# Kernel tuning notes

Measured on AMD Instinct MI355X. Metric: run time of the kernel, lower is better.

Reference implementation:

```python
import jax, jax.numpy as jnp
import numpy as np
from jax import lax

IMG_DIM = 512
D_MODEL = 768
N_LAYER = 12
D_INNER = 2 * D_MODEL          # 1536
D_STATE = 16
D_CONV = 4
DT_RANK = (D_MODEL + 15) // 16 # 48
BATCH = 4
SEQ = 256


def setup_inputs() -> dict:
    key = jax.random.key(0)
    ks = jax.random.split(key, 16)
    s = 0.02
    inp = {
        "frames_rep": jax.random.normal(ks[0], (BATCH, SEQ, IMG_DIM), jnp.float32),
        "fproj_w": jax.random.normal(ks[1], (IMG_DIM, D_MODEL), jnp.float32) * s,
        "fproj_b": jnp.zeros((D_MODEL,), jnp.float32),
        "norm_w": jnp.ones((N_LAYER, D_MODEL), jnp.float32),
        "in_w": jax.random.normal(ks[2], (N_LAYER, D_MODEL, 2 * D_INNER), jnp.float32) * s,
        "conv_w": jax.random.normal(ks[3], (N_LAYER, D_INNER, D_CONV), jnp.float32) * s,
        "conv_b": jnp.zeros((N_LAYER, D_INNER), jnp.float32),
        "xproj_w": jax.random.normal(ks[4], (N_LAYER, D_INNER, DT_RANK + 2 * D_STATE), jnp.float32) * s,
        "dt_w": jax.random.normal(ks[5], (N_LAYER, DT_RANK, D_INNER), jnp.float32) * s,
        "dt_b": jnp.full((N_LAYER, D_INNER), -2.0, jnp.float32),  # softplus(-2)~0.13
        "A_log": jnp.broadcast_to(jnp.log(jnp.arange(1, D_STATE + 1, dtype=jnp.float32)), (N_LAYER, D_INNER, D_STATE)) * jnp.ones((N_LAYER, D_INNER, 1)),
        "D_param": jnp.ones((N_LAYER, D_INNER), jnp.float32),
        "out_w": jax.random.normal(ks[6], (N_LAYER, D_INNER, D_MODEL), jnp.float32) * s,
        "normf_w": jnp.ones((D_MODEL,), jnp.float32),
    }
    return inp


def _rmsnorm(x, w, eps=1e-5):
    return x * lax.rsqrt(jnp.mean(x * x, axis=-1, keepdims=True) + eps) * w


def _mamba_layer(x, in_w, conv_w, conv_b, xproj_w, dt_w, dt_b, A_log, D_param, out_w):
    # x: (B, L, D_MODEL)
    B, L, _ = x.shape
    xz = x @ in_w                                  # (B, L, 2*di)
    xi, res = jnp.split(xz, 2, axis=-1)            # each (B, L, di)
    # depthwise causal conv over time
    xc = jnp.transpose(xi, (0, 2, 1))              # (B, di, L)
    xc = lax.conv_general_dilated(
        xc, conv_w[:, None, :], (1,), [(D_CONV - 1, 0)],
        feature_group_count=D_INNER)
    xi = jax.nn.silu(jnp.transpose(xc + conv_b[None, :, None], (0, 2, 1)))
    # input-dependent SSM parameters
    x_dbl = xi @ xproj_w                           # (B, L, dt_rank + 2n)
    delta = x_dbl[..., :DT_RANK]
    Bm = x_dbl[..., DT_RANK:DT_RANK + D_STATE]     # (B, L, n)
    Cm = x_dbl[..., DT_RANK + D_STATE:]            # (B, L, n)
    delta = jax.nn.softplus(delta @ dt_w + dt_b)   # (B, L, di)
    A = -jnp.exp(A_log)                            # (di, n)
    deltaA = jnp.exp(delta[..., None] * A)                               # (B, L, di, n)
    deltaBu = delta[..., None] * Bm[:, :, None, :] * xi[..., None]       # (B, L, di, n)

    def step(h, inp):
        dA, dBu, c = inp
        h = dA * h + dBu                           # (B, di, n)
        y = jnp.einsum('bdn,bn->bd', h, c)
        return h, y

    xs = (deltaA.transpose(1, 0, 2, 3), deltaBu.transpose(1, 0, 2, 3), Cm.transpose(1, 0, 2))
    h0 = jnp.zeros((B, D_INNER, D_STATE), x.dtype)
    _, ys = lax.scan(step, h0, xs)                 # (L, B, di)
    y = ys.transpose(1, 0, 2) + xi * D_param
    y = y * jax.nn.silu(res)
    return y @ out_w                               # (B, L, D_MODEL)


def reference(frames_rep, fproj_w, fproj_b, norm_w, in_w, conv_w, conv_b,
              xproj_w, dt_w, dt_b, A_log, D_param, out_w, normf_w):
    h = jax.nn.relu(frames_rep @ fproj_w + fproj_b)       # (B, L, D_MODEL)
    for i in range(N_LAYER):
        h = h + _mamba_layer(_rmsnorm(h, norm_w[i]), in_w[i], conv_w[i], conv_b[i],
                             xproj_w[i], dt_w[i], dt_b[i], A_log[i], D_param[i], out_w[i])
    return _rmsnorm(h, normf_w)
```

## Files before the change

kernel.cpp:

```cpp
#include <hip/hip_runtime.h>
#include <hip/hip_bf16.h>
#include <cmath>

#define IMG_DIM 512
#define D_MODEL 768
#define N_LAYER 12
#define D_INNER 1536
#define D_STATE 16
#define D_CONV 4
#define DT_RANK 48
#define BATCH 4
#define SEQ 256
#define M_TOK (BATCH * SEQ)
#define XPROJ_N (DT_RANK + 2 * D_STATE)
#define KSPLIT 8
#define NCHUNK 16
#define CLEN 16
#define LOG2E 1.4426950408889634f

typedef __attribute__((ext_vector_type(8))) short bf16x8;
typedef __attribute__((ext_vector_type(4))) float f32x4;
typedef __hip_bfloat16 bf16;

__device__ __forceinline__ float softplus_f(float v) {
    return v > 20.f ? v : log1pf(expf(v));
}
__device__ __forceinline__ float b2f(bf16 v) { return __bfloat162float(v); }

__global__ __launch_bounds__(256) void wcvt_t_k(
    const float* __restrict__ W, bf16* __restrict__ WT, int K, int N)
{
    __shared__ float tile[32][33];
    W  += (size_t)blockIdx.z * K * N;
    WT += (size_t)blockIdx.z * K * N;
    const int tx = threadIdx.x & 31;
    const int ty4 = (threadIdx.x >> 5) * 4;
    const int n0 = blockIdx.x * 32, k0 = blockIdx.y * 32;
    #pragma unroll
    for (int r = 0; r < 4; ++r)
        tile[ty4 + r][tx] = (n0 + tx < N)
            ? W[(size_t)(k0 + ty4 + r) * N + n0 + tx] : 0.f;
    __syncthreads();
    #pragma unroll
    for (int r = 0; r < 4; ++r)
        if (n0 + ty4 + r < N)
            WT[(size_t)(n0 + ty4 + r) * K + k0 + tx] =
                __float2bfloat16(tile[tx][ty4 + r]);
}

__global__ __launch_bounds__(256) void cvt_bf16_k(
    const float* __restrict__ in, bf16* __restrict__ out, int n)
{
    int i = blockIdx.x * 256 + threadIdx.x;
    if (i < n) out[i] = __float2bfloat16(in[i]);
}

__global__ __launch_bounds__(256) void dtw_cvt_k(
    const float* __restrict__ dt_w, bf16* __restrict__ dtwT)
{
    int idx = blockIdx.x * 256 + threadIdx.x;
    int k = idx & 63;
    int n = (idx >> 6) % D_INNER;
    int l = idx / (64 * D_INNER);
    dtwT[idx] = (k < DT_RANK)
        ? __float2bfloat16(dt_w[((size_t)l * DT_RANK + k) * D_INNER + n])
        : bf16(0.f);
}

__global__ __launch_bounds__(256) void a2_k(
    const float* __restrict__ A_log, float* __restrict__ A2)
{
    int idx = blockIdx.x * 256 + threadIdx.x;
    A2[idx] = -expf(A_log[idx]) * LOG2E;
}

template <int EPI, typename OT>
__global__ __launch_bounds__(256) void gemm_bf16(
    const bf16* __restrict__ A,
    const bf16* __restrict__ BT,
    OT* __restrict__ C, int ldc, int K,
    const float* __restrict__ bias)
{
    __shared__ __align__(16) char lds[2][16384];
    const int tid = threadIdx.x;
    const int lane = tid & 63;
    const int wid = tid >> 6;
    const int wr = wid >> 1, wc = wid & 1;
    const size_t rowBase = blockIdx.x * 64;
    const size_t colBase = blockIdx.y * 64;

    const int r0 = tid >> 3;
    const int cb0 = (tid & 7) * 16;
    const int wOffA = r0 * 128 + (cb0 ^ ((r0 & 7) << 4));
    const char* gA = (const char*)(A + rowBase * K);
    const char* gB = (const char*)(BT + colBase * K);
    const size_t rowByteOff = (size_t)r0 * K * 2 + cb0;

    const int lrow = lane & 15;
    const int kg = (lane >> 4) * 16;
    const int swz = (lane & 7) << 4;

    f32x4 acc[2][2] = {};

    const int nt = K >> 6;
    float4 ra0, ra1, rb0, rb1;

    ra0 = *(const float4*)(gA + rowByteOff);
    ra1 = *(const float4*)(gA + rowByteOff + (size_t)32 * K * 2);
    rb0 = *(const float4*)(gB + rowByteOff);
    rb1 = *(const float4*)(gB + rowByteOff + (size_t)32 * K * 2);
    *(float4*)(&lds[0][wOffA])        = ra0;
    *(float4*)(&lds[0][wOffA + 4096]) = ra1;
    *(float4*)(&lds[0][wOffA + 8192]) = rb0;
    *(float4*)(&lds[0][wOffA + 12288])= rb1;
    __syncthreads();

    for (int t = 0; t < nt; ++t) {
        const int cur = t & 1;
        if (t + 1 < nt) {
            size_t off = rowByteOff + (size_t)(t + 1) * 128;
            ra0 = *(const float4*)(gA + off);
            ra1 = *(const float4*)(gA + off + (size_t)32 * K * 2);
            rb0 = *(const float4*)(gB + off);
            rb1 = *(const float4*)(gB + off + (size_t)32 * K * 2);
        }
        #pragma unroll
        for (int kk = 0; kk < 2; ++kk) {
            const int col = (kk * 64 + kg) ^ swz;
            bf16x8 a0 = *(const bf16x8*)(&lds[cur][(wr * 32 +      lrow) * 128 + col]);
            bf16x8 a1 = *(const bf16x8*)(&lds[cur][(wr * 32 + 16 + lrow) * 128 + col]);
            bf16x8 b0 = *(const bf16x8*)(&lds[cur][8192 + (wc * 32 +      lrow) * 128 + col]);
            bf16x8 b1 = *(const bf16x8*)(&lds[cur][8192 + (wc * 32 + 16 + lrow) * 128 + col]);
            acc[0][0] = __builtin_amdgcn_mfma_f32_16x16x32_bf16(a0, b0, acc[0][0], 0, 0, 0);
            acc[0][1] = __builtin_amdgcn_mfma_f32_16x16x32_bf16(a0, b1, acc[0][1], 0, 0, 0);
            acc[1][0] = __builtin_amdgcn_mfma_f32_16x16x32_bf16(a1, b0, acc[1][0], 0, 0, 0);
            acc[1][1] = __builtin_amdgcn_mfma_f32_16x16x32_bf16(a1, b1, acc[1][1], 0, 0, 0);
        }
        if (t + 1 < nt) {
            const int nxt = cur ^ 1;
            *(float4*)(&lds[nxt][wOffA])        = ra0;
            *(float4*)(&lds[nxt][wOffA + 4096]) = ra1;
            *(float4*)(&lds[nxt][wOffA + 8192]) = rb0;
            *(float4*)(&lds[nxt][wOffA + 12288])= rb1;
        }
        __syncthreads();
    }

    const int mBase = (int)rowBase + wr * 32 + (lane >> 4) * 4;
    const int nBase = (int)colBase + wc * 32 + (lane & 15);
    #pragma unroll
    for (int i = 0; i < 2; ++i)
        #pragma unroll
        for (int j = 0; j < 2; ++j)
            #pragma unroll
            for (int rg = 0; rg < 4; ++rg) {
                int cc = nBase + j * 16;
                size_t idx = (size_t)(mBase + i * 16 + rg) * ldc + cc;
                float v = acc[i][j][rg];
                if (EPI == 0) {
                    C[idx] = (OT)v;
                } else if (EPI == 1) {
                    v += bias[cc];
                    C[idx] = (OT)(v > 0.f ? v : 0.f);
                } else if (EPI == 2) {
                    v += bias[cc];
                    C[idx] = (OT)softplus_f(v);
                } else {
                    C[idx] += v;
                }
            }
}

__global__ __launch_bounds__(256) void xproj_gemm_k(
    const bf16* __restrict__ xc_bf,
    const bf16* __restrict__ xprojT,
    float* __restrict__ part)
{
    const int lane = threadIdx.x & 63;
    const int w = threadIdx.x >> 6;
    const int m0 = blockIdx.x * 64 + w * 16;
    const int ks = blockIdx.y;
    const int KS = D_INNER / KSPLIT;
    const int k0 = ks * KS;

    const int arow = m0 + (lane & 15);
    const int kgrp = (lane >> 4) * 8;

    f32x4 acc[5] = {};
    const bf16* ap = xc_bf + (size_t)arow * D_INNER + kgrp;
    const bf16* bp = xprojT + (size_t)(lane & 15) * D_INNER + kgrp;

    for (int k = k0; k < k0 + KS; k += 32) {
        bf16x8 a = *(const bf16x8*)(ap + k);
        #pragma unroll
        for (int f = 0; f < 5; ++f) {
            bf16x8 b = *(const bf16x8*)(bp + (size_t)f * 16 * D_INNER + k);
            acc[f] = __builtin_amdgcn_mfma_f32_16x16x32_bf16(a, b, acc[f], 0, 0, 0);
        }
    }

    float* out = part + (size_t)ks * M_TOK * XPROJ_N;
    const int rowb = blockIdx.x * 64 + w * 16 + (lane >> 4) * 4;
    #pragma unroll
    for (int f = 0; f < 5; ++f)
        #pragma unroll
        for (int rg = 0; rg < 4; ++rg)
            out[(size_t)(rowb + rg) * XPROJ_N + f * 16 + (lane & 15)] = acc[f][rg];
}

__global__ __launch_bounds__(256) void xproj_reduce_k(
    const float* __restrict__ part, float* __restrict__ xdbl,
    bf16* __restrict__ dtin)
{
    int idx = blockIdx.x * 256 + threadIdx.x;
    float s = 0.f;
    #pragma unroll
    for (int p = 0; p < KSPLIT; ++p)
        s += part[(size_t)p * M_TOK * XPROJ_N + idx];
    xdbl[idx] = s;
    int col = idx % XPROJ_N;
    int row = idx / XPROJ_N;
    if (col < DT_RANK)
        dtin[(size_t)row * 64 + col] = __float2bfloat16(s);
}

template <typename OT>
__global__ __launch_bounds__(256) void rmsnorm_k(
    const float* __restrict__ x, const float* __restrict__ w,
    OT* __restrict__ o)
{
    const int row = blockIdx.x;
    const float* xr = x + (size_t)row * D_MODEL;
    float v[3];
    float s = 0.f;
    #pragma unroll
    for (int i = 0; i < 3; ++i) {
        v[i] = xr[threadIdx.x + i * 256];
        s = fmaf(v[i], v[i], s);
    }
    #pragma unroll
    for (int off = 32; off > 0; off >>= 1) s += __shfl_down(s, off);
    __shared__ float red[4];
    if ((threadIdx.x & 63) == 0) red[threadIdx.x >> 6] = s;
    __syncthreads();
    float tot = red[0] + red[1] + red[2] + red[3];
    float r = rsqrtf(tot * (1.f / D_MODEL) + 1e-5f);
    OT* orow = o + (size_t)row * D_MODEL;
    #pragma unroll
    for (int i = 0; i < 3; ++i) {
        int c = threadIdx.x + i * 256;
        orow[c] = (OT)(v[i] * r * w[c]);
    }
}

__global__ __launch_bounds__(256) void conv_silu_k(
    const bf16* __restrict__ xz, const float* __restrict__ cw,
    const float* __restrict__ cb, bf16* __restrict__ xc_bf)
{
    int idx = blockIdx.x * 256 + threadIdx.x;
    int d = idx % D_INNER;
    int bt = idx / D_INNER;
    int t = bt & (SEQ - 1);
    int b = bt >> 8;
    float acc = cb[d];
    #pragma unroll
    for (int k = 0; k < 4; ++k) {
        int tt = t - 3 + k;
        if (tt >= 0)
            acc = fmaf(b2f(xz[(size_t)(b * SEQ + tt) * (2 * D_INNER) + d]),
                       cw[d * 4 + k], acc);
    }
    float sig = 1.f / (1.f + expf(-acc));
    xc_bf[idx] = __float2bfloat16(acc * sig);
}

__global__ __launch_bounds__(256) void scan_part_k(
    const bf16* __restrict__ delta,
    const bf16* __restrict__ xc,
    const float* __restrict__ xdbl,
    const float* __restrict__ A2,
    const float* __restrict__ D_param,
    float* __restrict__ cumdv,
    float* __restrict__ ypart,
    float* __restrict__ hpart)
{
    __shared__ float sBC[CLEN][32];
    const int tid = threadIdx.x;
    const int dgrp  = blockIdx.x % 6;
    const int chunk = (blockIdx.x / 6) & (NCHUNK - 1);
    const int b     = blockIdx.x / (6 * NCHUNK);
    const int d  = dgrp * 256 + tid;
    const int t0 = chunk * CLEN;

    {
        int r = tid >> 5, c = tid & 31;
        sBC[r][c]     = xdbl[(size_t)(b * SEQ + t0 + r) * XPROJ_N + DT_RANK + c];
        sBC[r + 8][c] = xdbl[(size_t)(b * SEQ + t0 + r + 8) * XPROJ_N + DT_RANK + c];
    }

    float a2[16];
    {
        const float4* ap = (const float4*)(A2 + (size_t)d * 16);
        #pragma unroll
        for (int q = 0; q < 4; ++q) {
            float4 v = ap[q];
            a2[q * 4 + 0] = v.x; a2[q * 4 + 1] = v.y;
            a2[q * 4 + 2] = v.z; a2[q * 4 + 3] = v.w;
        }
    }
    const float Dp = D_param[d];

    const size_t base = (size_t)(b * SEQ + t0) * D_INNER + d;
    const bf16* dp = delta + base;
    const bf16* up = xc + base;

    float dvv[CLEN], uvv[CLEN];
    #pragma unroll
    for (int s = 0; s < CLEN; ++s) {
        dvv[s] = b2f(dp[(size_t)s * D_INNER]);
        uvv[s] = b2f(up[(size_t)s * D_INNER]);
    }
    __syncthreads();

    float h[16];
    #pragma unroll
    for (int n = 0; n < 16; ++n) h[n] = 0.f;
    float cum = 0.f;

    #pragma unroll
    for (int s = 0; s < CLEN; ++s) {
        float dv = dvv[s], u = uvv[s];
        cum += dv;
        cumdv[base + (size_t)s * D_INNER] = cum;
        float du = dv * u;
        float yv = 0.f;
        #pragma unroll
        for (int n = 0; n < 16; ++n) {
            float dA = exp2f(dv * a2[n]);
            h[n] = fmaf(dA, h[n], du * sBC[s][n]);
            yv = fmaf(h[n], sBC[s][16 + n], yv);
        }
        ypart[base + (size_t)s * D_INNER] = fmaf(u, Dp, yv);
    }

    float4* hp = (float4*)(hpart + (((size_t)b * NCHUNK + chunk) * D_INNER + d) * 16);
    #pragma unroll
    for (int q = 0; q < 4; ++q) {
        float4 v;
        v.x = h[q * 4 + 0]; v.y = h[q * 4 + 1];
        v.z = h[q * 4 + 2]; v.w = h[q * 4 + 3];
        hp[q] = v;
    }
}

__global__ __launch_bounds__(256) void scan_pref_k(
    const float* __restrict__ cumdv,
    const float* __restrict__ hpart,
    const float* __restrict__ A2,
    float* __restrict__ hinb)
{
    int idx = blockIdx.x * 256 + threadIdx.x;
    int n = idx & 15;
    int r = idx >> 4;
    int d = r % D_INNER;
    int b = r / D_INNER;
    float a2 = A2[(size_t)d * 16 + n];
    float hin = 0.f;
    #pragma unroll
    for (int c = 0; c < NCHUNK; ++c) {
        hinb[(((size_t)b * NCHUNK + c) * D_INNER + d) * 16 + n] = hin;
        float sdv = cumdv[(size_t)(b * SEQ + c * CLEN + CLEN - 1) * D_INNER + d];
        float hp  = hpart[(((size_t)b * NCHUNK + c) * D_INNER + d) * 16 + n];
        hin = fmaf(hin, exp2f(a2 * sdv), hp);
    }
}

__global__ __launch_bounds__(256) void scan_fix_k(
    const float* __restrict__ ypart,
    const float* __restrict__ cumdv,
    const float* __restrict__ xdbl,
    const bf16* __restrict__ xz,
    const float* __restrict__ A2,
    const float* __restrict__ hinb,
    bf16* __restrict__ y)
{
    __shared__ float sC[16];
    int idx = blockIdx.x * 256 + threadIdx.x;
    int d = idx % D_INNER;
    int bt = idx / D_INNER;
    int t = bt & (SEQ - 1);
    int b = bt >> 8;
    int chunk = t >> 4;

    if (threadIdx.x < 16)
        sC[threadIdx.x] = xdbl[(size_t)bt * XPROJ_N + DT_RANK + D_STATE + threadIdx.x];
    __syncthreads();

    float cum = cumdv[idx];
    float yp  = ypart[idx];
    float res = b2f(xz[(size_t)bt * 2 * D_INNER + D_INNER + d]);

    const float4* hp = (const float4*)(hinb + (((size_t)b * NCHUNK + chunk) * D_INNER + d) * 16);
    const float4* ap = (const float4*)(A2 + (size_t)d * 16);

    float corr = 0.f;
    #pragma unroll
    for (int q = 0; q < 4; ++q) {
        float4 hv = hp[q];
        float4 av = ap[q];
        corr = fmaf(exp2f(av.x * cum) * hv.x, sC[q * 4 + 0], corr);
        corr = fmaf(exp2f(av.y * cum) * hv.y, sC[q * 4 + 1], corr);
        corr = fmaf(exp2f(av.z * cum) * hv.z, sC[q * 4 + 2], corr);
        corr = fmaf(exp2f(av.w * cum) * hv.w, sC[q * 4 + 3], corr);
    }
    float sr = res / (1.f + expf(-res));
    y[idx] = __float2bfloat16((yp + corr) * sr);
}

extern "C" void kernel_launch(void* const* d_in, const int* in_sizes, int n_in,
                              void* d_out, int out_size, void* d_ws, size_t ws_size,
                              hipStream_t stream)
{
    const float* frames  = (const float*)d_in[0];
    const float* fproj_w = (const float*)d_in[1];
    const float* fproj_b = (const float*)d_in[2];
    const float* norm_w  = (const float*)d_in[3];
    const float* in_w    = (const float*)d_in[4];
    const float* conv_w  = (const float*)d_in[5];
    const float* conv_b  = (const float*)d_in[6];
    const float* xproj_w = (const float*)d_in[7];
    const float* dt_w    = (const float*)d_in[8];
    const float* dt_b    = (const float*)d_in[9];
    const float* A_log   = (const float*)d_in[10];
    const float* D_param = (const float*)d_in[11];
    const float* out_w   = (const float*)d_in[12];
    const float* normf_w = (const float*)d_in[13];

    char* ws = (char*)d_ws;
    float* h      = (float*)ws;        ws += (size_t)M_TOK * D_MODEL * 4;
    float* xdbl   = (float*)ws;        ws += (size_t)M_TOK * XPROJ_N * 4;
    float* part   = (float*)ws;        ws += (size_t)KSPLIT * M_TOK * XPROJ_N * 4;
    float* cumdv  = (float*)ws;        ws += (size_t)M_TOK * D_INNER * 4;
    float* ypartb = (float*)ws;        ws += (size_t)M_TOK * D_INNER * 4;
    float* hpartb = (float*)ws;        ws += (size_t)BATCH * NCHUNK * D_INNER * 16 * 4;
    float* hinb   = (float*)ws;        ws += (size_t)BATCH * NCHUNK * D_INNER * 16 * 4;
    float* A2all  = (float*)ws;        ws += (size_t)N_LAYER * D_INNER * 16 * 4;
    bf16* xz_bf   = (bf16*)ws;         ws += (size_t)M_TOK * 2 * D_INNER * 2;
    bf16* xc_bf   = (bf16*)ws;         ws += (size_t)M_TOK * D_INNER * 2;
    bf16* delta_bf= (bf16*)ws;         ws += (size_t)M_TOK * D_INNER * 2;
    bf16* x_bf    = (bf16*)ws;         ws += (size_t)M_TOK * D_MODEL * 2;
    bf16* y_bf    = (bf16*)ws;         ws += (size_t)M_TOK * D_INNER * 2;
    bf16* dtin    = (bf16*)ws;         ws += (size_t)M_TOK * 64 * 2;
    bf16* fr_bf   = (bf16*)ws;         ws += (size_t)M_TOK * IMG_DIM * 2;
    bf16* fp_wT   = (bf16*)ws;         ws += (size_t)D_MODEL * IMG_DIM * 2;
    bf16* in_wT   = (bf16*)ws;         ws += (size_t)N_LAYER * 2 * D_INNER * D_MODEL * 2;
    bf16* out_wT  = (bf16*)ws;         ws += (size_t)N_LAYER * D_MODEL * D_INNER * 2;
    bf16* xprojT  = (bf16*)ws;         ws += (size_t)N_LAYER * XPROJ_N * D_INNER * 2;
    bf16* dt_wT   = (bf16*)ws;         ws += (size_t)N_LAYER * D_INNER * 64 * 2;

    dim3 blk(256);

    hipMemsetAsync(dtin, 0, (size_t)M_TOK * 64 * 2, stream);
    cvt_bf16_k<<<(M_TOK * IMG_DIM) / 256, blk, 0, stream>>>(
        frames, fr_bf, M_TOK * IMG_DIM);
    wcvt_t_k<<<dim3(D_MODEL / 32, IMG_DIM / 32, 1), blk, 0, stream>>>(
        fproj_w, fp_wT, IMG_DIM, D_MODEL);
    wcvt_t_k<<<dim3(2 * D_INNER / 32, D_MODEL / 32, N_LAYER), blk, 0, stream>>>(
        in_w, in_wT, D_MODEL, 2 * D_INNER);
    wcvt_t_k<<<dim3(D_MODEL / 32, D_INNER / 32, N_LAYER), blk, 0, stream>>>(
        out_w, out_wT, D_INNER, D_MODEL);
    wcvt_t_k<<<dim3((XPROJ_N + 31) / 32, D_INNER / 32, N_LAYER), blk, 0, stream>>>(
        xproj_w, xprojT, D_INNER, XPROJ_N);
    dtw_cvt_k<<<(N_LAYER * D_INNER * 64) / 256, blk, 0, stream>>>(dt_w, dt_wT);
    a2_k<<<(N_LAYER * D_INNER * 16) / 256, blk, 0, stream>>>(A_log, A2all);

    gemm_bf16<1, float><<<dim3(M_TOK / 64, D_MODEL / 64), blk, 0, stream>>>(
        fr_bf, fp_wT, h, D_MODEL, IMG_DIM, fproj_b);

    for (int i = 0; i < N_LAYER; ++i) {
        const bf16* in_wTi   = in_wT  + (size_t)i * 2 * D_INNER * D_MODEL;
        const bf16* out_wTi  = out_wT + (size_t)i * D_MODEL * D_INNER;
        const bf16* xprojTi  = xprojT + (size_t)i * XPROJ_N * D_INNER;
        const bf16* dt_wTi   = dt_wT  + (size_t)i * D_INNER * 64;
        const float* A2i     = A2all  + (size_t)i * D_INNER * 16;
        const float* conv_wi = conv_w + (size_t)i * D_INNER * D_CONV;
        const float* conv_bi = conv_b + (size_t)i * D_INNER;
        const float* dt_bi   = dt_b   + (size_t)i * D_INNER;
        const float* D_parami= D_param+ (size_t)i * D_INNER;
        const float* norm_wi = norm_w + (size_t)i * D_MODEL;

        rmsnorm_k<bf16><<<M_TOK, blk, 0, stream>>>(h, norm_wi, x_bf);
        gemm_bf16<0, bf16><<<dim3(M_TOK / 64, (2 * D_INNER) / 64), blk, 0, stream>>>(
            x_bf, in_wTi, xz_bf, 2 * D_INNER, D_MODEL, nullptr);
        conv_silu_k<<<(M_TOK * D_INNER) / 256, blk, 0, stream>>>(
            xz_bf, conv_wi, conv_bi, xc_bf);
        xproj_gemm_k<<<dim3(M_TOK / 64, KSPLIT), blk, 0, stream>>>(
            xc_bf, xprojTi, part);
        xproj_reduce_k<<<(M_TOK * XPROJ_N) / 256, blk, 0, stream>>>(
            part, xdbl, dtin);
        gemm_bf16<2, bf16><<<dim3(M_TOK / 64, D_INNER / 64), blk, 0, stream>>>(
            dtin, dt_wTi, delta_bf, D_INNER, 64, dt_bi);
        scan_part_k<<<BATCH * NCHUNK * (D_INNER / 256), blk, 0, stream>>>(
            delta_bf, xc_bf, xdbl, A2i, D_parami, cumdv, ypartb, hpartb);
        scan_pref_k<<<(BATCH * D_INNER * 16) / 256, blk, 0, stream>>>(
            cumdv, hpartb, A2i, hinb);
        scan_fix_k<<<(M_TOK * D_INNER) / 256, blk, 0, stream>>>(
            ypartb, cumdv, xdbl, xz_bf, A2i, hinb, y_bf);
        gemm_bf16<3, float><<<dim3(M_TOK / 64, D_MODEL / 64), blk, 0, stream>>>(
            y_bf, out_wTi, h, D_MODEL, D_INNER, nullptr);
    }

    rmsnorm_k<float><<<M_TOK, blk, 0, stream>>>(h, normf_w, (float*)d_out);
}
```

Before: 1.307 ms.

## Fuse dt projection into scan, vectorize conv, use direct global-to-LDS loads in GEMM

Removes the separate dt GEMM, dtin buffer and dt_w conversion by computing the dt projection plus softplus in fp32 inside scan_part_k from xdbl rows staged in shared memory. The causal conv+SiLU kernel now handles 8 channels per thread with vector loads and stores. The bf16 GEMM loads tiles straight into LDS via global_load_lds, dropping the register staging step. The tradeoff is extra scalar FMAs and dt_w global reads in every scan block.

```diff
diff --git a/kernel.cpp b/kernel.cpp
--- a/kernel.cpp
+++ b/kernel.cpp
@@ -19,6 +19,7 @@
 #define LOG2E 1.4426950408889634f
 
 typedef __attribute__((ext_vector_type(8))) short bf16x8;
+typedef __attribute__((ext_vector_type(8))) unsigned short u16x8;
 typedef __attribute__((ext_vector_type(4))) float f32x4;
 typedef __hip_bfloat16 bf16;
 
@@ -26,6 +27,16 @@
     return v > 20.f ? v : log1pf(expf(v));
 }
 __device__ __forceinline__ float b2f(bf16 v) { return __bfloat162float(v); }
+__device__ __forceinline__ float us2f(unsigned short v) {
+    return __uint_as_float(((unsigned)v) << 16);
+}
+
+__device__ __forceinline__ void gl_lds16(const char* g, char* l) {
+    __builtin_amdgcn_global_load_lds(
+        (const __attribute__((address_space(1))) unsigned int*)g,
+        (__attribute__((address_space(3))) unsigned int*)l,
+        16, 0, 0);
+}
 
 __global__ __launch_bounds__(256) void wcvt_t_k(
     const float* __restrict__ W, bf16* __restrict__ WT, int K, int N)
@@ -53,18 +64,6 @@
 {
     int i = blockIdx.x * 256 + threadIdx.x;
     if (i < n) out[i] = __float2bfloat16(in[i]);
-}
-
-__global__ __launch_bounds__(256) void dtw_cvt_k(
-    const float* __restrict__ dt_w, bf16* __restrict__ dtwT)
-{
-    int idx = blockIdx.x * 256 + threadIdx.x;
-    int k = idx & 63;
-    int n = (idx >> 6) % D_INNER;
-    int l = idx / (64 * D_INNER);
-    dtwT[idx] = (k < DT_RANK)
-        ? __float2bfloat16(dt_w[((size_t)l * DT_RANK + k) * D_INNER + n])
-        : bf16(0.f);
 }
 
 __global__ __launch_bounds__(256) void a2_k(
@@ -91,38 +90,37 @@
 
     const int r0 = tid >> 3;
     const int cb0 = (tid & 7) * 16;
-    const int wOffA = r0 * 128 + (cb0 ^ ((r0 & 7) << 4));
+    const int slot = tid * 16;
+    const size_t gOffSw = (size_t)r0 * K * 2 + (cb0 ^ ((r0 & 7) << 4));
+    const size_t aStep = (size_t)32 * K * 2;
     const char* gA = (const char*)(A + rowBase * K);
     const char* gB = (const char*)(BT + colBase * K);
-    const size_t rowByteOff = (size_t)r0 * K * 2 + cb0;
 
     const int lrow = lane & 15;
     const int kg = (lane >> 4) * 16;
     const int swz = (lane & 7) << 4;
 
     f32x4 acc[2][2] = {};
-
     const int nt = K >> 6;
-    float4 ra0, ra1, rb0, rb1;
-
-    ra0 = *(const float4*)(gA + rowByteOff);
-    ra1 = *(const float4*)(gA + rowByteOff + (size_t)32 * K * 2);
-    rb0 = *(const float4*)(gB + rowByteOff);
-    rb1 = *(const float4*)(gB + rowByteOff + (size_t)32 * K * 2);
-    *(float4*)(&lds[0][wOffA])        = ra0;
-    *(float4*)(&lds[0][wOffA + 4096]) = ra1;
-    *(float4*)(&lds[0][wOffA + 8192]) = rb0;
-    *(float4*)(&lds[0][wOffA + 12288])= rb1;
+
+    {
+        char* L = &lds[0][0];
+        gl_lds16(gA + gOffSw,          L + slot);
+        gl_lds16(gA + gOffSw + aStep,  L + 4096 + slot);
+        gl_lds16(gB + gOffSw,          L + 8192 + slot);
+        gl_lds16(gB + gOffSw + aStep,  L + 12288 + slot);
+    }
     __syncthreads();
 
     for (int t = 0; t < nt; ++t) {
         const int cur = t & 1;
         if (t + 1 < nt) {
-            size_t off = rowByteOff + (size_t)(t + 1) * 128;
-            ra0 = *(const float4*)(gA + off);
-            ra1 = *(const float4*)(gA + off + (size_t)32 * K * 2);
-            rb0 = *(const float4*)(gB + off);
-            rb1 = *(const float4*)(gB + off + (size_t)32 * K * 2);
+            char* L = &lds[cur ^ 1][0];
+            size_t go = gOffSw + (size_t)(t + 1) * 128;
+            gl_lds16(gA + go,          L + slot);
+            gl_lds16(gA + go + aStep,  L + 4096 + slot);
+            gl_lds16(gB + go,          L + 8192 + slot);
+            gl_lds16(gB + go + aStep,  L + 12288 + slot);
         }
         #pragma unroll
         for (int kk = 0; kk < 2; ++kk) {
@@ -135,13 +133,6 @@
             acc[0][1] = __builtin_amdgcn_mfma_f32_16x16x32_bf16(a0, b1, acc[0][1], 0, 0, 0);
             acc[1][0] = __builtin_amdgcn_mfma_f32_16x16x32_bf16(a1, b0, acc[1][0], 0, 0, 0);
             acc[1][1] = __builtin_amdgcn_mfma_f32_16x16x32_bf16(a1, b1, acc[1][1], 0, 0, 0);
-        }
-        if (t + 1 < nt) {
-            const int nxt = cur ^ 1;
-            *(float4*)(&lds[nxt][wOffA])        = ra0;
-            *(float4*)(&lds[nxt][wOffA + 4096]) = ra1;
-            *(float4*)(&lds[nxt][wOffA + 8192]) = rb0;
-            *(float4*)(&lds[nxt][wOffA + 12288])= rb1;
         }
         __syncthreads();
     }
@@ -162,9 +153,6 @@
                 } else if (EPI == 1) {
                     v += bias[cc];
                     C[idx] = (OT)(v > 0.f ? v : 0.f);
-                } else if (EPI == 2) {
-                    v += bias[cc];
-                    C[idx] = (OT)softplus_f(v);
                 } else {
                     C[idx] += v;
                 }
@@ -209,8 +197,7 @@
 }
 
 __global__ __launch_bounds__(256) void xproj_reduce_k(
-    const float* __restrict__ part, float* __restrict__ xdbl,
-    bf16* __restrict__ dtin)
+    const float* __restrict__ part, float* __restrict__ xdbl)
 {
     int idx = blockIdx.x * 256 + threadIdx.x;
     float s = 0.f;
@@ -218,10 +205,6 @@
     for (int p = 0; p < KSPLIT; ++p)
         s += part[(size_t)p * M_TOK * XPROJ_N + idx];
     xdbl[idx] = s;
-    int col = idx % XPROJ_N;
-    int row = idx / XPROJ_N;
-    if (col < DT_RANK)
-        dtin[(size_t)row * 64 + col] = __float2bfloat16(s);
 }
 
 template <typename OT>
@@ -257,34 +240,60 @@
     const bf16* __restrict__ xz, const float* __restrict__ cw,
     const float* __restrict__ cb, bf16* __restrict__ xc_bf)
 {
-    int idx = blockIdx.x * 256 + threadIdx.x;
-    int d = idx % D_INNER;
-    int bt = idx / D_INNER;
+    int v = blockIdx.x * 256 + threadIdx.x;
+    int d8 = (v * 8) % D_INNER;
+    int bt = (v * 8) / D_INNER;
     int t = bt & (SEQ - 1);
     int b = bt >> 8;
-    float acc = cb[d];
+
+    float acc[8];
+    {
+        const float4* cbp = (const float4*)(cb + d8);
+        float4 c0 = cbp[0], c1 = cbp[1];
+        acc[0] = c0.x; acc[1] = c0.y; acc[2] = c0.z; acc[3] = c0.w;
+        acc[4] = c1.x; acc[5] = c1.y; acc[6] = c1.z; acc[7] = c1.w;
+    }
+    float4 wv[8];
+    #pragma unroll
+    for (int j = 0; j < 8; ++j)
+        wv[j] = *(const float4*)(cw + (size_t)(d8 + j) * 4);
+
     #pragma unroll
     for (int k = 0; k < 4; ++k) {
         int tt = t - 3 + k;
-        if (tt >= 0)
-            acc = fmaf(b2f(xz[(size_t)(b * SEQ + tt) * (2 * D_INNER) + d]),
-                       cw[d * 4 + k], acc);
-    }
-    float sig = 1.f / (1.f + expf(-acc));
-    xc_bf[idx] = __float2bfloat16(acc * sig);
+        if (tt >= 0) {
+            u16x8 xv = *(const u16x8*)(xz + (size_t)(b * SEQ + tt) * (2 * D_INNER) + d8);
+            #pragma unroll
+            for (int j = 0; j < 8; ++j) {
+                float wk = (k == 0) ? wv[j].x : (k == 1) ? wv[j].y
+                         : (k == 2) ? wv[j].z : wv[j].w;
+                acc[j] = fmaf(us2f(xv[j]), wk, acc[j]);
+            }
+        }
+    }
+
+    __align__(16) bf16 ob[8];
+    #pragma unroll
+    for (int j = 0; j < 8; ++j) {
+        float a = acc[j];
+        float s = a / (1.f + expf(-a));
+        ob[j] = __float2bfloat16(s);
+    }
+    *(uint4*)(xc_bf + (size_t)v * 8) = *(const uint4*)ob;
 }
 
 __global__ __launch_bounds__(256) void scan_part_k(
-    const bf16* __restrict__ delta,
     const bf16* __restrict__ xc,
     const float* __restrict__ xdbl,
+    const float* __restrict__ dt_w,
+    const float* __restrict__ dt_b,
     const float* __restrict__ A2,
     const float* __restrict__ D_param,
     float* __restrict__ cumdv,
     float* __restrict__ ypart,
     float* __restrict__ hpart)
 {
-    __shared__ float sBC[CLEN][32];
+    __shared__ float sXD[CLEN][XPROJ_N];
     const int tid = threadIdx.x;
     const int dgrp  = blockIdx.x % 6;
     const int chunk = (blockIdx.x / 6) & (NCHUNK - 1);
@@ -292,10 +301,11 @@
     const int d  = dgrp * 256 + tid;
     const int t0 = chunk * CLEN;
 
-    {
-        int r = tid >> 5, c = tid & 31;
-        sBC[r][c]     = xdbl[(size_t)(b * SEQ + t0 + r) * XPROJ_N + DT_RANK + c];
-        sBC[r + 8][c] = xdbl[(size_t)(b * SEQ + t0 + r + 8) * XPROJ_N + DT_RANK + c];
+    #pragma unroll
+    for (int j = 0; j < 5; ++j) {
+        int idx = tid + j * 256;
+        int r = idx / XPROJ_N, c = idx - r * XPROJ_N;
+        sXD[r][c] = xdbl[(size_t)(b * SEQ + t0 + r) * XPROJ_N + c];
     }
 
     float a2[16];
@@ -303,24 +313,40 @@
         const float4* ap = (const float4*)(A2 + (size_t)d * 16);
         #pragma unroll
         for (int q = 0; q < 4; ++q) {
-            float4 v = ap[q];
-            a2[q * 4 + 0] = v.x; a2[q * 4 + 1] = v.y;
-            a2[q * 4 + 2] = v.z; a2[q * 4 + 3] = v.w;
+            float4 vv = ap[q];
+            a2[q * 4 + 0] = vv.x; a2[q * 4 + 1] = vv.y;
+            a2[q * 4 + 2] = vv.z; a2[q * 4 + 3] = vv.w;
         }
     }
     const float Dp = D_param[d];
+    const float bias = dt_b[d];
 
     const size_t base = (size_t)(b * SEQ + t0) * D_INNER + d;
-    const bf16* dp = delta + base;
-    const bf16* up = xc + base;
-
-    float dvv[CLEN], uvv[CLEN];
-    #pragma unroll
-    for (int s = 0; s < CLEN; ++s) {
-        dvv[s] = b2f(dp[(size_t)s * D_INNER]);
-        uvv[s] = b2f(up[(size_t)s * D_INNER]);
-    }
+    float uvv[CLEN];
+    #pragma unroll
+    for (int s = 0; s < CLEN; ++s)
+        uvv[s] = b2f(xc[base + (size_t)s * D_INNER]);
+
     __syncthreads();
+
+    float acc[CLEN];
+    #pragma unroll
+    for (int s = 0; s < CLEN; ++s) acc[s] = bias;
+    #pragma unroll
+    for (int kq = 0; kq < DT_RANK / 4; ++kq) {
+        float w0 = dt_w[(size_t)(kq * 4 + 0) * D_INNER + d];
+        float w1 = dt_w[(size_t)(kq * 4 + 1) * D_INNER + d];
+        float w2 = dt_w[(size_t)(kq * 4 + 2) * D_INNER + d];
+        float w3 = dt_w[(size_t)(kq * 4 + 3) * D_INNER + d];
+        #pragma unroll
+        for (int s = 0; s < CLEN; ++s) {
+            float4 xv = *(const float4*)&sXD[s][kq * 4];
+            acc[s] = fmaf(xv.x, w0, acc[s]);
+            acc[s] = fmaf(xv.y, w1, acc[s]);
+            acc[s] = fmaf(xv.z, w2, acc[s]);
+            acc[s] = fmaf(xv.w, w3, acc[s]);
+        }
+    }
 
     float h[16];
     #pragma unroll
@@ -329,16 +355,26 @@
 
     #pragma unroll
     for (int s = 0; s < CLEN; ++s) {
-        float dv = dvv[s], u = uvv[s];
+        float dv = softplus_f(acc[s]);
+        float u = uvv[s];
         cum += dv;
         cumdv[base + (size_t)s * D_INNER] = cum;
         float du = dv * u;
+        float Bv[16], Cv[16];
+        *(float4*)&Bv[0]  = *(const float4*)&sXD[s][48];
+        *(float4*)&Bv[4]  = *(const float4*)&sXD[s][52];
+        *(float4*)&Bv[8]  = *(const float4*)&sXD[s][56];
+        *(float4*)&Bv[12] = *(const float4*)&sXD[s][60];
+        *(float4*)&Cv[0]  = *(const float4*)&sXD[s][64];
+        *(float4*)&Cv[4]  = *(const float4*)&sXD[s][68];
+        *(float4*)&Cv[8]  = *(const float4*)&sXD[s][72];
+        *(float4*)&Cv[12] = *(const float4*)&sXD[s][76];
         float yv = 0.f;
         #pragma unroll
         for (int n = 0; n < 16; ++n) {
             float dA = exp2f(dv * a2[n]);
-            h[n] = fmaf(dA, h[n], du * sBC[s][n]);
-            yv = fmaf(h[n], sBC[s][16 + n], yv);
+            h[n] = fmaf(dA, h[n], du * Bv[n]);
+            yv = fmaf(h[n], Cv[n], yv);
         }
         ypart[base + (size_t)s * D_INNER] = fmaf(u, Dp, yv);
     }
@@ -346,10 +382,10 @@
     float4* hp = (float4*)(hpart + (((size_t)b * NCHUNK + chunk) * D_INNER + d) * 16);
     #pragma unroll
     for (int q = 0; q < 4; ++q) {
-        float4 v;
-        v.x = h[q * 4 + 0]; v.y = h[q * 4 + 1];
-        v.z = h[q * 4 + 2]; v.w = h[q * 4 + 3];
-        hp[q] = v;
+        float4 vv;
+        vv.x = h[q * 4 + 0]; vv.y = h[q * 4 + 1];
+        vv.z = h[q * 4 + 2]; vv.w = h[q * 4 + 3];
+        hp[q] = vv;
     }
 }
 
@@ -447,20 +483,16 @@
     float* A2all  = (float*)ws;        ws += (size_t)N_LAYER * D_INNER * 16 * 4;
     bf16* xz_bf   = (bf16*)ws;         ws += (size_t)M_TOK * 2 * D_INNER * 2;
     bf16* xc_bf   = (bf16*)ws;         ws += (size_t)M_TOK * D_INNER * 2;
-    bf16* delta_bf= (bf16*)ws;         ws += (size_t)M_TOK * D_INNER * 2;
     bf16* x_bf    = (bf16*)ws;         ws += (size_t)M_TOK * D_MODEL * 2;
     bf16* y_bf    = (bf16*)ws;         ws += (size_t)M_TOK * D_INNER * 2;
-    bf16* dtin    = (bf16*)ws;         ws += (size_t)M_TOK * 64 * 2;
     bf16* fr_bf   = (bf16*)ws;         ws += (size_t)M_TOK * IMG_DIM * 2;
     bf16* fp_wT   = (bf16*)ws;         ws += (size_t)D_MODEL * IMG_DIM * 2;
     bf16* in_wT   = (bf16*)ws;         ws += (size_t)N_LAYER * 2 * D_INNER * D_MODEL * 2;
     bf16* out_wT  = (bf16*)ws;         ws += (size_t)N_LAYER * D_MODEL * D_INNER * 2;
     bf16* xprojT  = (bf16*)ws;         ws += (size_t)N_LAYER * XPROJ_N * D_INNER * 2;
-    bf16* dt_wT   = (bf16*)ws;         ws += (size_t)N_LAYER * D_INNER * 64 * 2;
 
     dim3 blk(256);
 
-    hipMemsetAsync(dtin, 0, (size_t)M_TOK * 64 * 2, stream);
     cvt_bf16_k<<<(M_TOK * IMG_DIM) / 256, blk, 0, stream>>>(
         frames, fr_bf, M_TOK * IMG_DIM);
     wcvt_t_k<<<dim3(D_MODEL / 32, IMG_DIM / 32, 1), blk, 0, stream>>>(
@@ -471,7 +503,6 @@
         out_w, out_wT, D_INNER, D_MODEL);
     wcvt_t_k<<<dim3((XPROJ_N + 31) / 32, D_INNER / 32, N_LAYER), blk, 0, stream>>>(
         xproj_w, xprojT, D_INNER, XPROJ_N);
-    dtw_cvt_k<<<(N_LAYER * D_INNER * 64) / 256, blk, 0, stream>>>(dt_w, dt_wT);
     a2_k<<<(N_LAYER * D_INNER * 16) / 256, blk, 0, stream>>>(A_log, A2all);
 
     gemm_bf16<1, float><<<dim3(M_TOK / 64, D_MODEL / 64), blk, 0, stream>>>(
@@ -481,10 +512,10 @@
         const bf16* in_wTi   = in_wT  + (size_t)i * 2 * D_INNER * D_MODEL;
         const bf16* out_wTi  = out_wT + (size_t)i * D_MODEL * D_INNER;
         const bf16* xprojTi  = xprojT + (size_t)i * XPROJ_N * D_INNER;
-        const bf16* dt_wTi   = dt_wT  + (size_t)i * D_INNER * 64;
         const float* A2i     = A2all  + (size_t)i * D_INNER * 16;
         const float* conv_wi = conv_w + (size_t)i * D_INNER * D_CONV;
         const float* conv_bi = conv_b + (size_t)i * D_INNER;
+        const float* dt_wi   = dt_w   + (size_t)i * DT_RANK * D_INNER;
         const float* dt_bi   = dt_b   + (size_t)i * D_INNER;
         const float* D_parami= D_param+ (size_t)i * D_INNER;
         const float* norm_wi = norm_w + (size_t)i * D_MODEL;
@@ -492,16 +523,14 @@
         rmsnorm_k<bf16><<<M_TOK, blk, 0, stream>>>(h, norm_wi, x_bf);
         gemm_bf16<0, bf16><<<dim3(M_TOK / 64, (2 * D_INNER) / 64), blk, 0, stream>>>(
             x_bf, in_wTi, xz_bf, 2 * D_INNER, D_MODEL, nullptr);
-        conv_silu_k<<<(M_TOK * D_INNER) / 256, blk, 0, stream>>>(
+        conv_silu_k<<<(M_TOK * D_INNER / 8) / 256, blk, 0, stream>>>(
             xz_bf, conv_wi, conv_bi, xc_bf);
         xproj_gemm_k<<<dim3(M_TOK / 64, KSPLIT), blk, 0, stream>>>(
             xc_bf, xprojTi, part);
         xproj_reduce_k<<<(M_TOK * XPROJ_N) / 256, blk, 0, stream>>>(
-            part, xdbl, dtin);
-        gemm_bf16<2, bf16><<<dim3(M_TOK / 64, D_INNER / 64), blk, 0, stream>>>(
-            dtin, dt_wTi, delta_bf, D_INNER, 64, dt_bi);
+            part, xdbl);
         scan_part_k<<<BATCH * NCHUNK * (D_INNER / 256), blk, 0, stream>>>(
-            delta_bf, xc_bf, xdbl, A2i, D_parami, cumdv, ypartb, hpartb);
+            xc_bf, xdbl, dt_wi, dt_bi, A2i, D_parami, cumdv, ypartb, hpartb);
         scan_pref_k<<<(BATCH * D_INNER * 16) / 256, blk, 0, stream>>>(
             cumdv, hpartb, A2i, hinb);
         scan_fix_k<<<(M_TOK * D_INNER) / 256, blk, 0, stream>>>(
```

Result: slower. 2.235 ms (+71.0%).
